# Kernel tuning notes

Measured on AMD Instinct MI355X. Metric: run time of the kernel, lower is better.

Reference implementation:

```python
import jax, jax.numpy as jnp
from jax import lax
import numpy as np

N = 10000      # nodes
T = 60         # lookback window
F = 16         # features per timestep
HL = 256       # lstm hidden dim
GH = 8         # gat heads
GC = 64        # gat out channels per head
GD = GH * GC   # 512 concat dim
FH = 512       # fusion hidden
E = 320000     # edges (before self loops)


def _lstm_layer(x, w_ih, w_hh, b_ih, b_hh):
    # x: [T, N, in] -> hidden sequence [T, N, HL]; torch gate order i,f,g,o
    n = x.shape[1]
    h0 = jnp.zeros((n, HL), x.dtype)
    def step(carry, xt):
        h, c = carry
        g = xt @ w_ih.T + h @ w_hh.T + b_ih + b_hh
        i, f, gg, o = jnp.split(g, 4, axis=-1)
        c = jax.nn.sigmoid(f) * c + jax.nn.sigmoid(i) * jnp.tanh(gg)
        h = jax.nn.sigmoid(o) * jnp.tanh(c)
        return (h, c), h
    _, hs = lax.scan(step, (h0, h0), x)
    return hs


def _gatv2(x, src, dst, ea, wl, bl, wr, br, we, att, bias):
    # GATv2Conv (concat=True, edge_dim=1, negative_slope=0.2); self loops already in src/dst/ea
    n = x.shape[0]
    xl = (x @ wl + bl).reshape(n, GH, GC)   # lin_l (source / x_j)
    xr = (x @ wr + br).reshape(n, GH, GC)   # lin_r (target / x_i)
    ee = (ea @ we).reshape(-1, GH, GC)      # lin_edge (bias=False)
    m = jax.nn.leaky_relu(xl[src] + xr[dst] + ee, 0.2)      # [E', GH, GC]
    logits = jnp.einsum('ehc,hc->eh', m, att)               # [E', GH]
    mx = jax.ops.segment_max(logits, dst, num_segments=n)
    ex = jnp.exp(logits - mx[dst])
    den = jax.ops.segment_sum(ex, dst, num_segments=n)
    alpha = ex / den[dst]                                   # softmax over in-edges per node
    out = jax.ops.segment_sum(xl[src] * alpha[..., None], dst, num_segments=n)
    return out.reshape(n, GD) + bias


def setup_inputs():
    key = jax.random.key(0)
    ks = jax.random.split(key, 20)
    f32 = jnp.float32
    def nrm(k, shp, fan):
        return jax.random.normal(k, shp, f32) * (1.0 / np.sqrt(fan))
    return {
        "x_seq": jax.random.normal(ks[0], (N, T, F), f32),
        "edge_index": jax.random.randint(ks[1], (2, E), 0, N, jnp.int32),
        "edge_attr": jax.random.uniform(ks[2], (E, 1), dtype=f32),
        "w_ih0": nrm(ks[3], (4 * HL, F), HL), "w_hh0": nrm(ks[4], (4 * HL, HL), HL),
        "b_ih0": jnp.zeros((4 * HL,), f32), "b_hh0": jnp.zeros((4 * HL,), f32),
        "w_ih1": nrm(ks[5], (4 * HL, HL), HL), "w_hh1": nrm(ks[6], (4 * HL, HL), HL),
        "b_ih1": jnp.zeros((4 * HL,), f32), "b_hh1": jnp.zeros((4 * HL,), f32),
        "g0_wl": nrm(ks[7], (HL, GD), HL), "g0_bl": jnp.zeros((GD,), f32),
        "g0_wr": nrm(ks[8], (HL, GD), HL), "g0_br": jnp.zeros((GD,), f32),
        "g0_we": nrm(ks[9], (1, GD), 1),
        "g0_att": nrm(ks[10], (GH, GC), GC), "g0_bias": jnp.zeros((GD,), f32),
        "g1_wl": nrm(ks[11], (GD, GD), GD), "g1_bl": jnp.zeros((GD,), f32),
        "g1_wr": nrm(ks[12], (GD, GD), GD), "g1_br": jnp.zeros((GD,), f32),
        "g1_we": nrm(ks[13], (1, GD), 1),
        "g1_att": nrm(ks[14], (GH, GC), GC), "g1_bias": jnp.zeros((GD,), f32),
        "fc1_w": nrm(ks[15], (HL + GD, FH), HL + GD), "fc1_b": jnp.zeros((FH,), f32),
        "fc2_w": nrm(ks[16], (FH, 1), FH), "fc2_b": jnp.zeros((1,), f32),
    }


def reference(x_seq, edge_index, edge_attr,
              w_ih0, w_hh0, b_ih0, b_hh0, w_ih1, w_hh1, b_ih1, b_hh1,
              g0_wl, g0_bl, g0_wr, g0_br, g0_we, g0_att, g0_bias,
              g1_wl, g1_bl, g1_wr, g1_br, g1_we, g1_att, g1_bias,
              fc1_w, fc1_b, fc2_w, fc2_b):
    # 2-layer LSTM encoder, take last timestep hidden (dropout off: eval mode)
    xt = jnp.transpose(x_seq, (1, 0, 2))            # [T, N, F]
    h1 = _lstm_layer(xt, w_ih0, w_hh0, b_ih0, b_hh0)
    h2 = _lstm_layer(h1, w_ih1, w_hh1, b_ih1, b_hh1)
    node = h2[-1]                                    # [N, HL]
    # add self loops; fill edge_attr for loops with mean (PyG default fill_value='mean')
    loop = jnp.arange(N, dtype=edge_index.dtype)
    src = jnp.concatenate([edge_index[0], loop])
    dst = jnp.concatenate([edge_index[1], loop])
    ea = jnp.concatenate([edge_attr, jnp.broadcast_to(edge_attr.mean(axis=0), (N, 1))], axis=0)
    g = jax.nn.elu(_gatv2(node, src, dst, ea, g0_wl, g0_bl, g0_wr, g0_br, g0_we, g0_att, g0_bias))
    g = jax.nn.elu(_gatv2(g, src, dst, ea, g1_wl, g1_bl, g1_wr, g1_br, g1_we, g1_att, g1_bias))
    fused = jnp.concatenate([node, g], axis=1)       # [N, HL+GD]
    h = jax.nn.relu(fused @ fc1_w + fc1_b)
    return h @ fc2_w + fc2_b                         # [N, 1]
```

## Files before the change

### kernel.cpp

```cpp
#include <hip/hip_runtime.h>

#define DEV __device__ __forceinline__

typedef _Float16 f16;
typedef _Float16 f16x8 __attribute__((ext_vector_type(8)));
typedef _Float16 f16x2 __attribute__((ext_vector_type(2)));
typedef float f32x4 __attribute__((ext_vector_type(4)));

DEV float sigmoidf_(float x) { return 1.0f / (1.0f + __expf(-x)); }
DEV float tanhf2_(float x)   { return 1.0f - 2.0f / (__expf(2.0f * x) + 1.0f); }

DEV void load_lds16(const void* g, void* l) {
    __builtin_amdgcn_global_load_lds(
        (const __attribute__((address_space(1))) char*)(const char*)g,
        (__attribute__((address_space(3))) char*)(unsigned int)(unsigned long long)(char*)l,
        16, 0, 0);
}

DEV int swz(int row, int ck) { return ck ^ (row & 3) ^ ((row >> 2) & 3); }

__global__ void prep_w0_kernel(const float* __restrict__ wih,
                               const float* __restrict__ whh,
                               f16* __restrict__ dst) {
    int idx = blockIdx.x * 256 + threadIdx.x;
    if (idx >= 1024 * 320) return;
    int rd = idx / 320, k = idx - rd * 320;
    int T = rd >> 7, p = rd & 127;
    int u = T * 32 + ((p >> 6) & 1) * 16 + (p & 15);
    int g = (p >> 4) & 3;
    int src = g * 256 + u;
    float v;
    if (k < 16)        v = wih[src * 16 + k];
    else if (k < 272)  v = whh[src * 256 + (k - 16)];
    else               v = 0.f;
    dst[idx] = (f16)v;
}

__global__ void prep_w1_kernel(const float* __restrict__ wih,
                               const float* __restrict__ whh,
                               f16* __restrict__ dst) {
    int idx = blockIdx.x * 256 + threadIdx.x;
    if (idx >= 1024 * 512) return;
    int rd = idx >> 9, k = idx & 511;
    int T = rd >> 7, p = rd & 127;
    int u = T * 32 + ((p >> 6) & 1) * 16 + (p & 15);
    int g = (p >> 4) & 3;
    int src = g * 256 + u;
    float v = (k < 256) ? wih[src * 256 + k] : whh[src * 256 + (k - 256)];
    dst[idx] = (f16)v;
}

__global__ void prep_bias4_kernel(const float* __restrict__ bi,
                                  const float* __restrict__ bh,
                                  float* __restrict__ dst) {
    int idx = blockIdx.x * 256 + threadIdx.x;
    if (idx >= 1024) return;
    int u = idx >> 2, g = idx & 3;
    dst[idx] = bi[g * 256 + u] + bh[g * 256 + u];
}

__global__ void prep_wt_kernel(const float* __restrict__ src, f16* __restrict__ dst,
                               int K, int N) {
    int idx = blockIdx.x * 256 + threadIdx.x;
    if (idx >= K * N) return;
    int n = idx / K, k = idx - n * K;
    dst[idx] = (f16)src[(size_t)k * N + n];
}

__global__ void prep_x0_kernel(const float* __restrict__ x_seq, f16* __restrict__ A0,
                               int Nn) {
    int idx = blockIdx.x * 256 + threadIdx.x;
    if (idx >= Nn * 16) return;
    int m = idx >> 4, f = idx & 15;
    A0[(size_t)m * 320 + f] = (f16)x_seq[(size_t)m * 960 + f];
}

DEV void lstm_step_core(
    f16* __restrict__ sA, f16* __restrict__ sB,
    int bx, int by,
    const f16* __restrict__ A, int lda, int K,
    const f16* __restrict__ Wt,
    const float* __restrict__ bias4,
    float* __restrict__ c_state,
    f16* __restrict__ hA, int ldhA, int offhA,
    f16* __restrict__ hB, int ldhB, int offhB,
    const float* __restrict__ xsrc, int tnext,
    int M)
{
    const int tid = threadIdx.x;
    const int w = tid >> 6, lane = tid & 63;
    const int m0 = bx * 128, n0 = by * 128;
    const int arow = lane >> 2;
    const int achk = swz(arow, lane & 3) * 8;
    const int frow = lane & 15, l4 = lane >> 4;
    const int fsl = swz(frow, l4) * 8;
    const int wr = (w >> 1) * 64, wc = (w & 1) * 64;

    const int u = by * 32 + (w & 1) * 16 + (lane & 15);
    const int rbase = m0 + wr + (lane >> 4) * 4;
    float cold[4][4];
#pragma unroll
    for (int i = 0; i < 4; ++i)
#pragma unroll
        for (int r = 0; r < 4; ++r)
            cold[i][r] = c_state[(size_t)(rbase + i * 16 + r) * 256 + u];

    f32x4 acc[4][4] = {};

    for (int k0 = 0; k0 < K; k0 += 64) {
        __syncthreads();
#pragma unroll
        for (int half = 0; half < 2; ++half) {
#pragma unroll
            for (int c = 0; c < 2; ++c) {
                int R = c * 64 + w * 16;
                load_lds16(A + (size_t)(m0 + R + arow) * lda + k0 + half * 32 + achk,
                           sA + half * 4096 + R * 32);
                load_lds16(Wt + (size_t)(n0 + R + arow) * K + k0 + half * 32 + achk,
                           sB + half * 4096 + R * 32);
            }
        }
        __syncthreads();
#pragma unroll
        for (int half = 0; half < 2; ++half) {
            f16x8 af[4], bf[4];
#pragma unroll
            for (int i = 0; i < 4; ++i)
                af[i] = *(const f16x8*)&sA[half * 4096 + (wr + i * 16 + frow) * 32 + fsl];
#pragma unroll
            for (int j = 0; j < 4; ++j)
                bf[j] = *(const f16x8*)&sB[half * 4096 + (wc + j * 16 + frow) * 32 + fsl];
#pragma unroll
            for (int i = 0; i < 4; ++i)
#pragma unroll
                for (int j = 0; j < 4; ++j)
                    acc[i][j] = __builtin_amdgcn_mfma_f32_16x16x32_f16(af[i], bf[j], acc[i][j], 0, 0, 0);
        }
    }

    const float4 bb = *(const float4*)&bias4[u * 4];
#pragma unroll
    for (int i = 0; i < 4; ++i) {
#pragma unroll
        for (int r = 0; r < 4; ++r) {
            int m = rbase + i * 16 + r;
            if (m < M) {
                float gi = sigmoidf_(acc[i][0][r] + bb.x);
                float gf = sigmoidf_(acc[i][1][r] + bb.y);
                float gg = tanhf2_(acc[i][2][r] + bb.z);
                float go = sigmoidf_(acc[i][3][r] + bb.w);
                float cn = gf * cold[i][r] + gi * gg;
                c_state[(size_t)m * 256 + u] = cn;
                f16 h = (f16)(go * tanhf2_(cn));
                hA[(size_t)m * ldhA + offhA + u] = h;
                if (hB) hB[(size_t)m * ldhB + offhB + u] = h;
            }
        }
    }
    if (xsrc && by == 0) {
        int row = tid >> 1, fb = (tid & 1) * 8;
        int m = m0 + row;
        if (m < M) {
            const float* xp = xsrc + (size_t)m * 960 + tnext * 16 + fb;
            f16* dp = hB + (size_t)m * ldhB + fb;
#pragma unroll
            for (int q = 0; q < 8; ++q) dp[q] = (f16)xp[q];
        }
    }
}

__global__ __launch_bounds__(256) void lstm_mfma_kernel(
    const f16* __restrict__ A, int lda, int K,
    const f16* __restrict__ Wt, const float* __restrict__ bias4,
    float* __restrict__ c_state,
    f16* __restrict__ hA, int ldhA, int offhA,
    f16* __restrict__ hB, int ldhB, int offhB,
    const float* __restrict__ xsrc, int tnext, int M, int mtiles)
{
    __shared__ __align__(16) f16 sA[2 * 4096];
    __shared__ __align__(16) f16 sB[2 * 4096];
    const int l = blockIdx.x;
    const int xcd = l & 7, q = l >> 3;
    const int y = q & 7, xhi = q >> 3;
    const int x = xhi * 8 + xcd;
    if (x >= mtiles) return;
    lstm_step_core(sA, sB, x, y, A, lda, K, Wt, bias4, c_state,
                   hA, ldhA, offhA, hB, ldhB, offhB, xsrc, tnext, M);
}

__global__ __launch_bounds__(256) void lstm_dual_kernel(
    const f16* __restrict__ A1, const f16* __restrict__ W1t,
    const float* __restrict__ b41, float* __restrict__ c1,
    f16* __restrict__ h1A, int ldh1A, int offh1A,
    const f16* __restrict__ A0, const f16* __restrict__ W0t,
    const float* __restrict__ b40, float* __restrict__ c0,
    f16* __restrict__ h0A, int ldh0A, int offh0A,
    f16* __restrict__ h0B, int ldh0B, int offh0B,
    const float* __restrict__ xsrc, int tnext, int M, int mtiles)
{
    __shared__ __align__(16) f16 sA[2 * 4096];
    __shared__ __align__(16) f16 sB[2 * 4096];
    const int l = blockIdx.x;
    const int xcd = l & 7, q = l >> 3;
    const int yz = q & 15, xhi = q >> 4;
    const int x = xhi * 8 + xcd;
    if (x >= mtiles) return;
    const int y = yz & 7, z = yz >> 3;
    if (z == 0)
        lstm_step_core(sA, sB, x, y, A1, 512, 512, W1t, b41, c1,
                       h1A, ldh1A, offh1A, nullptr, 0, 0, nullptr, 0, M);
    else
        lstm_step_core(sA, sB, x, y, A0, 320, 320, W0t, b40, c0,
                       h0A, ldh0A, offh0A, h0B, ldh0B, offh0B, xsrc, tnext, M);
}

__global__ __launch_bounds__(256) void gemm16_kernel(
    const f16* __restrict__ A, int lda,
    const f16* __restrict__ Bt, int K,
    const float* __restrict__ bias,
    f16* __restrict__ C16, float* __restrict__ C32, int ldc,
    int act, int M)
{
    __shared__ __align__(16) f16 sA[128 * 32];
    __shared__ __align__(16) f16 sB[128 * 32];
    const int tid = threadIdx.x;
    const int w = tid >> 6, lane = tid & 63;
    const int m0 = blockIdx.x * 128, n0 = blockIdx.y * 128;
    const int arow = lane >> 2;
    const int achk = swz(arow, lane & 3) * 8;
    const int frow = lane & 15, l4 = lane >> 4;
    const int fsl = swz(frow, l4) * 8;
    const int wr = (w >> 1) * 64, wcn = (w & 1) * 64;

    f32x4 acc[4][4] = {};

    for (int k0 = 0; k0 < K; k0 += 32) {
        __syncthreads();
#pragma unroll
        for (int c = 0; c < 2; ++c) {
            int R = c * 64 + w * 16;
            load_lds16(A + (size_t)(m0 + R + arow) * lda + k0 + achk, sA + R * 32);
            load_lds16(Bt + (size_t)(n0 + R + arow) * K + k0 + achk, sB + R * 32);
        }
        __syncthreads();
        f16x8 af[4], bf[4];
#pragma unroll
        for (int i = 0; i < 4; ++i)
            af[i] = *(const f16x8*)&sA[(wr + i * 16 + frow) * 32 + fsl];
#pragma unroll
        for (int j = 0; j < 4; ++j)
            bf[j] = *(const f16x8*)&sB[(wcn + j * 16 + frow) * 32 + fsl];
#pragma unroll
        for (int i = 0; i < 4; ++i)
#pragma unroll
            for (int j = 0; j < 4; ++j)
                acc[i][j] = __builtin_amdgcn_mfma_f32_16x16x32_f16(af[i], bf[j], acc[i][j], 0, 0, 0);
    }

    const int rbase = m0 + wr + (lane >> 4) * 4;
#pragma unroll
    for (int i = 0; i < 4; ++i) {
#pragma unroll
        for (int r = 0; r < 4; ++r) {
            int m = rbase + i * 16 + r;
            if (m >= M) continue;
#pragma unroll
            for (int j = 0; j < 4; ++j) {
                int n = n0 + wcn + j * 16 + (lane & 15);
                float v = acc[i][j][r] + bias[n];
                if (act == 1) v = fmaxf(v, 0.f);
                if (C16) C16[(size_t)m * ldc + n] = (f16)v;
                else     C32[(size_t)m * ldc + n] = v;
            }
        }
    }
}

__global__ __launch_bounds__(256) void gemm16_dual_kernel(
    const f16* __restrict__ A, int lda,
    const f16* __restrict__ Btl, const f16* __restrict__ Btr, int K,
    const float* __restrict__ biasl, const float* __restrict__ biasr,
    f16* __restrict__ Cl, f16* __restrict__ Cr, int ldc, int M)
{
    __shared__ __align__(16) f16 sA[128 * 32];
    __shared__ __align__(16) f16 sB[128 * 32];
    const int side = blockIdx.y >> 2;
    const f16* Bt = side ? Btr : Btl;
    const float* bias = side ? biasr : biasl;
    f16* C16 = side ? Cr : Cl;
    const int tid = threadIdx.x;
    const int w = tid >> 6, lane = tid & 63;
    const int m0 = blockIdx.x * 128, n0 = (blockIdx.y & 3) * 128;
    const int arow = lane >> 2;
    const int achk = swz(arow, lane & 3) * 8;
    const int frow = lane & 15, l4 = lane >> 4;
    const int fsl = swz(frow, l4) * 8;
    const int wr = (w >> 1) * 64, wcn = (w & 1) * 64;

    f32x4 acc[4][4] = {};

    for (int k0 = 0; k0 < K; k0 += 32) {
        __syncthreads();
#pragma unroll
        for (int c = 0; c < 2; ++c) {
            int R = c * 64 + w * 16;
            load_lds16(A + (size_t)(m0 + R + arow) * lda + k0 + achk, sA + R * 32);
            load_lds16(Bt + (size_t)(n0 + R + arow) * K + k0 + achk, sB + R * 32);
        }
        __syncthreads();
        f16x8 af[4], bf[4];
#pragma unroll
        for (int i = 0; i < 4; ++i)
            af[i] = *(const f16x8*)&sA[(wr + i * 16 + frow) * 32 + fsl];
#pragma unroll
        for (int j = 0; j < 4; ++j)
            bf[j] = *(const f16x8*)&sB[(wcn + j * 16 + frow) * 32 + fsl];
#pragma unroll
        for (int i = 0; i < 4; ++i)
#pragma unroll
            for (int j = 0; j < 4; ++j)
                acc[i][j] = __builtin_amdgcn_mfma_f32_16x16x32_f16(af[i], bf[j], acc[i][j], 0, 0, 0);
    }

    const int rbase = m0 + wr + (lane >> 4) * 4;
#pragma unroll
    for (int i = 0; i < 4; ++i) {
#pragma unroll
        for (int r = 0; r < 4; ++r) {
            int m = rbase + i * 16 + r;
            if (m >= M) continue;
#pragma unroll
            for (int j = 0; j < 4; ++j) {
                int n = n0 + wcn + j * 16 + (lane & 15);
                float v = acc[i][j][r] + bias[n];
                C16[(size_t)m * ldc + n] = (f16)v;
            }
        }
    }
}

__global__ void mean_sum_kernel(const float* __restrict__ a, int n, float* __restrict__ out) {
    __shared__ float s[256];
    float loc = 0.f;
    for (int i = blockIdx.x * 256 + threadIdx.x; i < n; i += gridDim.x * 256) loc += a[i];
    s[threadIdx.x] = loc;
    __syncthreads();
    for (int off = 128; off; off >>= 1) {
        if (threadIdx.x < off) s[threadIdx.x] += s[threadIdx.x + off];
        __syncthreads();
    }
    if (threadIdx.x == 0) atomicAdd(out, s[0]);
}

__global__ void hist_kernel(const int* __restrict__ ei, int Ne, int Nn,
                            int* __restrict__ counts) {
    int e = blockIdx.x * 256 + threadIdx.x;
    if (e >= Ne + Nn) return;
    int d = (e < Ne) ? ei[Ne + e] : (e - Ne);
    atomicAdd(&counts[d], 1);
}

__global__ void scan_kernel(const int* __restrict__ counts, int* __restrict__ offsets, int n) {
    __shared__ int s[256];
    int tid = threadIdx.x;
    int chunk = (n + 255) / 256;
    int b = tid * chunk;
    int loc = 0;
    for (int j = 0; j < chunk; ++j) { int i = b + j; if (i < n) loc += counts[i]; }
    s[tid] = loc;
    __syncthreads();
    for (int off = 1; off < 256; off <<= 1) {
        int v = (tid >= off) ? s[tid - off] : 0;
        __syncthreads();
        s[tid] += v;
        __syncthreads();
    }
    int run = (tid == 0) ? 0 : s[tid - 1];
    for (int j = 0; j < chunk; ++j) {
        int i = b + j;
        if (i < n) { offsets[i] = run; run += counts[i]; }
    }
    if (tid == 255) offsets[n] = run;
}

__global__ void scatter_kernel(const int* __restrict__ ei, const float* __restrict__ ea,
                               const float* __restrict__ sump, float inv_ne, int Ne, int Nn,
                               int* __restrict__ cursor, int* __restrict__ src_sorted,
                               float* __restrict__ ea_sorted) {
    int e = blockIdx.x * 256 + threadIdx.x;
    if (e >= Ne + Nn) return;
    int s, d; float a;
    if (e < Ne) { s = ei[e]; d = ei[Ne + e]; a = ea[e]; }
    else        { s = e - Ne; d = s; a = sump[0] * inv_ne; }
    int pos = atomicAdd(&cursor[d], 1);
    src_sorted[pos] = s;
    ea_sorted[pos] = a;
}

__global__ __launch_bounds__(256) void gat_aggregate_kernel(
    const f16* __restrict__ xl, const f16* __restrict__ xr,
    const float* __restrict__ we, const float* __restrict__ att,
    const float* __restrict__ bias,
    const int* __restrict__ offsets, const int* __restrict__ src_sorted,
    const float* __restrict__ ea_sorted,
    float* __restrict__ logit_buf, f16* __restrict__ out, int ldo, int N)
{
    __shared__ float s_xr[512], s_we[512], s_att[512];
    __shared__ float s_wmax[32], s_mx[8], s_den[8], s_rden[8];
    __shared__ float s_alpha[256];
    __shared__ int s_src[32];
    const int i = blockIdx.x;
    const int tid = threadIdx.x;
    s_xr[tid]       = (float)xr[(size_t)i * 512 + tid];
    s_xr[tid + 256] = (float)xr[(size_t)i * 512 + tid + 256];
    s_we[tid] = we[tid]; s_we[tid + 256] = we[tid + 256];
    s_att[tid] = att[tid]; s_att[tid + 256] = att[tid + 256];
    if (tid < 8) s_den[tid] = 0.f;
    __syncthreads();

    const int beg = offsets[i], end = offsets[i + 1];
    const int w = tid >> 6, lane = tid & 63;

    float wm[4] = {-1e30f, -1e30f, -1e30f, -1e30f};
    for (int e = beg + w; e < end; e += 4) {
        int s = src_sorted[e];
        float a = ea_sorted[e];
        float part[4];
#pragma unroll
        for (int cc = 0; cc < 4; ++cc) {
            int col = cc * 128 + lane * 2;
            f16x2 xv = *(const f16x2*)&xl[(size_t)s * 512 + col];
            float v0 = (float)xv.x + s_xr[col]     + a * s_we[col];
            float v1 = (float)xv.y + s_xr[col + 1] + a * s_we[col + 1];
            v0 = (v0 > 0.f) ? v0 : 0.2f * v0;
            v1 = (v1 > 0.f) ? v1 : 0.2f * v1;
            part[cc] = v0 * s_att[col] + v1 * s_att[col + 1];
        }
#pragma unroll
        for (int off = 16; off; off >>= 1)
#pragma unroll
            for (int cc = 0; cc < 4; ++cc) part[cc] += __shfl_xor(part[cc], off);
        if ((lane & 31) == 0) {
            int hb = lane >> 5;
#pragma unroll
            for (int cc = 0; cc < 4; ++cc) {
                logit_buf[(size_t)e * 8 + 2 * cc + hb] = part[cc];
                wm[cc] = fmaxf(wm[cc], part[cc]);
            }
        }
    }
    if ((lane & 31) == 0) {
        int hb = lane >> 5;
#pragma unroll
        for (int cc = 0; cc < 4; ++cc) s_wmax[w * 8 + 2 * cc + hb] = wm[cc];
    }
    __syncthreads();
    if (tid < 8) {
        float m = fmaxf(fmaxf(s_wmax[tid], s_wmax[8 + tid]),
                        fmaxf(s_wmax[16 + tid], s_wmax[24 + tid]));
        s_mx[tid] = m;
    }
    __syncthreads();

    for (int e = beg + tid; e < end; e += 256) {
#pragma unroll
        for (int h = 0; h < 8; ++h) {
            float ex = __expf(logit_buf[(size_t)e * 8 + h] - s_mx[h]);
            logit_buf[(size_t)e * 8 + h] = ex;
            atomicAdd(&s_den[h], ex);
        }
    }
    __syncthreads();
    if (tid < 8) s_rden[tid] = 1.f / s_den[tid];
    __syncthreads();

    float acc0 = 0.f, acc1 = 0.f;
    const int c2 = tid * 2, hh = tid >> 5;
    for (int chunk = beg; chunk < end; chunk += 32) {
        int cnt = min(32, end - chunk);
        if (tid < cnt) s_src[tid] = src_sorted[chunk + tid];
        int eo = tid >> 3, hq = tid & 7;
        if (eo < cnt) s_alpha[tid] = logit_buf[(size_t)(chunk + eo) * 8 + hq] * s_rden[hq];
        __syncthreads();
        for (int j = 0; j < cnt; ++j) {
            int s = s_src[j];
            f16x2 xv = *(const f16x2*)&xl[(size_t)s * 512 + c2];
            float al = s_alpha[j * 8 + hh];
            acc0 += al * (float)xv.x;
            acc1 += al * (float)xv.y;
        }
        __syncthreads();
    }
    float v0 = acc0 + bias[c2];
    float v1 = acc1 + bias[c2 + 1];
    v0 = (v0 > 0.f) ? v0 : __expf(v0) - 1.f;
    v1 = (v1 > 0.f) ? v1 : __expf(v1) - 1.f;
    f16x2 ov; ov.x = (f16)v0; ov.y = (f16)v1;
    *(f16x2*)&out[(size_t)i * ldo + c2] = ov;
}

__global__ void fc2_kernel(const float* __restrict__ H, const float* __restrict__ w,
                           const float* __restrict__ b, float* __restrict__ out, int N) {
    int wv = threadIdx.x >> 6, lane = threadIdx.x & 63;
    int node = blockIdx.x * 4 + wv;
    if (node >= N) return;
    float s = 0.f;
#pragma unroll
    for (int j = 0; j < 8; ++j)
        s += H[(size_t)node * 512 + j * 64 + lane] * w[j * 64 + lane];
#pragma unroll
    for (int off = 32; off; off >>= 1) s += __shfl_xor(s, off, 64);
    if (lane == 0) out[node] = s + b[0];
}

extern "C" void kernel_launch(void* const* d_in, const int* in_sizes, int n_in,
                              void* d_out, int out_size, void* d_ws, size_t ws_size,
                              hipStream_t stream) {
    const float* x_seq     = (const float*)d_in[0];
    const int*   edge_index= (const int*)d_in[1];
    const float* edge_attr = (const float*)d_in[2];
    const float* w_ih0 = (const float*)d_in[3];
    const float* w_hh0 = (const float*)d_in[4];
    const float* b_ih0 = (const float*)d_in[5];
    const float* b_hh0 = (const float*)d_in[6];
    const float* w_ih1 = (const float*)d_in[7];
    const float* w_hh1 = (const float*)d_in[8];
    const float* b_ih1 = (const float*)d_in[9];
    const float* b_hh1 = (const float*)d_in[10];
    const float* g0_wl = (const float*)d_in[11];
    const float* g0_bl = (const float*)d_in[12];
    const float* g0_wr = (const float*)d_in[13];
    const float* g0_br = (const float*)d_in[14];
    const float* g0_we = (const float*)d_in[15];
    const float* g0_att= (const float*)d_in[16];
    const float* g0_bias=(const float*)d_in[17];
    const float* g1_wl = (const float*)d_in[18];
    const float* g1_bl = (const float*)d_in[19];
    const float* g1_wr = (const float*)d_in[20];
    const float* g1_br = (const float*)d_in[21];
    const float* g1_we = (const float*)d_in[22];
    const float* g1_att= (const float*)d_in[23];
    const float* g1_bias=(const float*)d_in[24];
    const float* fc1_w = (const float*)d_in[25];
    const float* fc1_b = (const float*)d_in[26];
    const float* fc2_w = (const float*)d_in[27];
    const float* fc2_b = (const float*)d_in[28];
    float* out = (float*)d_out;

    const int Nn = in_sizes[0] / (60 * 16);
    const int Ne = in_sizes[1] / 2;
    const int Etot = Ne + Nn;
    const int MT = (Nn + 127) / 128;
    const int Mpad = MT * 128;
    const int MTpad8 = ((MT + 7) / 8) * 8;

    size_t off = 0;
    auto alloc = [&](size_t bytes) -> void* {
        void* r = (char*)d_ws + off;
        off += (bytes + 255) & ~(size_t)255;
        return r;
    };
    f16* W0t   = (f16*)alloc((size_t)1024 * 320 * 2);
    f16* W1t   = (f16*)alloc((size_t)1024 * 512 * 2);
    float* b40 = (float*)alloc(1024 * 4);
    float* b41 = (float*)alloc(1024 * 4);
    f16* Wg0l  = (f16*)alloc((size_t)512 * 256 * 2);
    f16* Wg0r  = (f16*)alloc((size_t)512 * 256 * 2);
    f16* Wg1l  = (f16*)alloc((size_t)512 * 512 * 2);
    f16* Wg1r  = (f16*)alloc((size_t)512 * 512 * 2);
    f16* Wfc1  = (f16*)alloc((size_t)512 * 768 * 2);
    f16* A0b[2]; A0b[0] = (f16*)alloc((size_t)Mpad * 320 * 2);
                 A0b[1] = (f16*)alloc((size_t)Mpad * 320 * 2);
    f16* A1b[2]; A1b[0] = (f16*)alloc((size_t)Mpad * 512 * 2);
                 A1b[1] = (f16*)alloc((size_t)Mpad * 512 * 2);
    float* c0  = (float*)alloc((size_t)Mpad * 256 * 4);
    float* c1  = (float*)alloc((size_t)Mpad * 256 * 4);
    f16* fused = (f16*)alloc((size_t)Mpad * 768 * 2);
    f16* xlbuf = (f16*)alloc((size_t)Mpad * 512 * 2);
    f16* xrbuf = (f16*)alloc((size_t)Mpad * 512 * 2);
    f16* gbuf  = (f16*)alloc((size_t)Mpad * 512 * 2);
    float* hfc1= (float*)alloc((size_t)Mpad * 512 * 4);
    float* logit_buf = (float*)alloc((size_t)Etot * 8 * 4);
    int* counts  = (int*)alloc((size_t)Nn * 4);
    int* offsets = (int*)alloc((size_t)(Nn + 1) * 4);
    int* cursor  = (int*)alloc((size_t)Nn * 4);
    int* src_sorted = (int*)alloc((size_t)Etot * 4);
    float* ea_sorted = (float*)alloc((size_t)Etot * 4);
    float* meanp = (float*)alloc(256);

    prep_w0_kernel<<<dim3((1024 * 320 + 255) / 256), 256, 0, stream>>>(w_ih0, w_hh0, W0t);
    prep_w1_kernel<<<dim3((1024 * 512 + 255) / 256), 256, 0, stream>>>(w_ih1, w_hh1, W1t);
    prep_bias4_kernel<<<dim3(4), 256, 0, stream>>>(b_ih0, b_hh0, b40);
    prep_bias4_kernel<<<dim3(4), 256, 0, stream>>>(b_ih1, b_hh1, b41);
    prep_wt_kernel<<<dim3((256 * 512 + 255) / 256), 256, 0, stream>>>(g0_wl, Wg0l, 256, 512);
    prep_wt_kernel<<<dim3((256 * 512 + 255) / 256), 256, 0, stream>>>(g0_wr, Wg0r, 256, 512);
    prep_wt_kernel<<<dim3((512 * 512 + 255) / 256), 256, 0, stream>>>(g1_wl, Wg1l, 512, 512);
    prep_wt_kernel<<<dim3((512 * 512 + 255) / 256), 256, 0, stream>>>(g1_wr, Wg1r, 512, 512);
    prep_wt_kernel<<<dim3((768 * 512 + 255) / 256), 256, 0, stream>>>(fc1_w, Wfc1, 768, 512);
    hipMemsetAsync(A0b[0], 0, (size_t)Mpad * 320 * 2, stream);
    hipMemsetAsync(A0b[1], 0, (size_t)Mpad * 320 * 2, stream);
    hipMemsetAsync(A1b[0], 0, (size_t)Mpad * 512 * 2, stream);
    hipMemsetAsync(c0, 0, (size_t)Mpad * 256 * 4, stream);
    hipMemsetAsync(c1, 0, (size_t)Mpad * 256 * 4, stream);
    prep_x0_kernel<<<dim3((Nn * 16 + 255) / 256), 256, 0, stream>>>(x_seq, A0b[0], Nn);

    hipMemsetAsync(meanp, 0, 4, stream);
    hipMemsetAsync(counts, 0, (size_t)Nn * 4, stream);
    mean_sum_kernel<<<dim3(256), 256, 0, stream>>>(edge_attr, Ne, meanp);
    hist_kernel<<<dim3((Etot + 255) / 256), 256, 0, stream>>>(edge_index, Ne, Nn, counts);
    scan_kernel<<<dim3(1), 256, 0, stream>>>(counts, offsets, Nn);
    hipMemcpyAsync(cursor, offsets, (size_t)Nn * 4, hipMemcpyDeviceToDevice, stream);
    scatter_kernel<<<dim3((Etot + 255) / 256), 256, 0, stream>>>(
        edge_index, edge_attr, meanp, 1.0f / (float)Ne, Ne, Nn, cursor, src_sorted, ea_sorted);

    const int solo_grid = MTpad8 * 8;
    const int dual_grid = MTpad8 * 16;
    lstm_mfma_kernel<<<dim3(solo_grid), 256, 0, stream>>>(
        A0b[0], 320, 320, W0t, b40, c0,
        A1b[0], 512, 0,
        A0b[1], 320, 16,
        x_seq, 1, Nn, MT);
    for (int k = 0; k < 59; ++k) {
        lstm_dual_kernel<<<dim3(dual_grid), 256, 0, stream>>>(
            A1b[k & 1], W1t, b41, c1,
            A1b[(k + 1) & 1], 512, 256,
            A0b[(k + 1) & 1], W0t, b40, c0,
            A1b[(k + 1) & 1], 512, 0,
            A0b[k & 1], 320, 16,
            (k + 1 < 59) ? x_seq : nullptr, k + 2, Nn, MT);
    }
    lstm_mfma_kernel<<<dim3(solo_grid), 256, 0, stream>>>(
        A1b[1], 512, 512, W1t, b41, c1,
        fused, 768, 0,
        nullptr, 0, 0,
        nullptr, 0, Nn, MT);

    gemm16_dual_kernel<<<dim3(MT, 8), 256, 0, stream>>>(
        fused, 768, Wg0l, Wg0r, 256, g0_bl, g0_br, xlbuf, xrbuf, 512, Nn);
    gat_aggregate_kernel<<<dim3(Nn), 256, 0, stream>>>(
        xlbuf, xrbuf, g0_we, g0_att, g0_bias, offsets, src_sorted, ea_sorted,
        logit_buf, gbuf, 512, Nn);

    gemm16_dual_kernel<<<dim3(MT, 8), 256, 0, stream>>>(
        gbuf, 512, Wg1l, Wg1r, 512, g1_bl, g1_br, xlbuf, xrbuf, 512, Nn);
    gat_aggregate_kernel<<<dim3(Nn), 256, 0, stream>>>(
        xlbuf, xrbuf, g1_we, g1_att, g1_bias, offsets, src_sorted, ea_sorted,
        logit_buf, fused + 256, 768, Nn);

    gemm16_kernel<<<dim3(MT, 4), 256, 0, stream>>>(
        fused, 768, Wfc1, 768, fc1_b, nullptr, hfc1, 512, 1, Nn);
    fc2_kernel<<<dim3((Nn + 3) / 4), 256, 0, stream>>>(hfc1, fc2_w, fc2_b, out, Nn);
}
```

Before: 3.363 ms.

## Double-buffer LDS tiles to overlap global loads with MFMA in GEMM kernels

The LSTM step core and both FP16 GEMM kernels now use a two-stage LDS ping-pong over 32-wide K chunks. The next chunk's global→LDS loads are issued right after a single barrier, before computing on the current chunk, so load latency overlaps with MFMA work and there is one barrier per chunk instead of two. The cost is double the LDS footprint in the GEMM kernels, which may lower occupancy. Because the barrier also waits on outstanding vector memory, the overlap only covers one chunk of compute.

```diff
diff --git a/kernel.cpp b/kernel.cpp
--- a/kernel.cpp
+++ b/kernel.cpp
@@ -75,6 +75,37 @@
     A0[(size_t)m * 320 + f] = (f16)x_seq[(size_t)m * 960 + f];
 }
 
+DEV void tile_load_chunk(const f16* __restrict__ A, int lda,
+                         const f16* __restrict__ Bt, int K,
+                         int m0, int n0, int k0,
+                         f16* __restrict__ sA, f16* __restrict__ sB,
+                         int w, int arow, int achk)
+{
+#pragma unroll
+    for (int c = 0; c < 2; ++c) {
+        int R = c * 64 + w * 16;
+        load_lds16(A + (size_t)(m0 + R + arow) * lda + k0 + achk, sA + R * 32);
+        load_lds16(Bt + (size_t)(n0 + R + arow) * K + k0 + achk, sB + R * 32);
+    }
+}
+
+DEV void tile_compute_chunk(const f16* __restrict__ sA, const f16* __restrict__ sB,
+                            f32x4 (&acc)[4][4], int wr, int wc, int frow, int fsl)
+{
+    f16x8 af[4], bf[4];
+#pragma unroll
+    for (int i = 0; i < 4; ++i)
+        af[i] = *(const f16x8*)&sA[(wr + i * 16 + frow) * 32 + fsl];
+#pragma unroll
+    for (int j = 0; j < 4; ++j)
+        bf[j] = *(const f16x8*)&sB[(wc + j * 16 + frow) * 32 + fsl];
+#pragma unroll
+    for (int i = 0; i < 4; ++i)
+#pragma unroll
+        for (int j = 0; j < 4; ++j)
+            acc[i][j] = __builtin_amdgcn_mfma_f32_16x16x32_f16(af[i], bf[j], acc[i][j], 0, 0, 0);
+}
+
 DEV void lstm_step_core(
     f16* __restrict__ sA, f16* __restrict__ sB,
     int bx, int by,
@@ -106,36 +137,18 @@
             cold[i][r] = c_state[(size_t)(rbase + i * 16 + r) * 256 + u];
 
     f32x4 acc[4][4] = {};
-
-    for (int k0 = 0; k0 < K; k0 += 64) {
-        __syncthreads();
-#pragma unroll
-        for (int half = 0; half < 2; ++half) {
-#pragma unroll
-            for (int c = 0; c < 2; ++c) {
-                int R = c * 64 + w * 16;
-                load_lds16(A + (size_t)(m0 + R + arow) * lda + k0 + half * 32 + achk,
-                           sA + half * 4096 + R * 32);
-                load_lds16(Wt + (size_t)(n0 + R + arow) * K + k0 + half * 32 + achk,
-                           sB + half * 4096 + R * 32);
-            }
-        }
-        __syncthreads();
-#pragma unroll
-        for (int half = 0; half < 2; ++half) {
-            f16x8 af[4], bf[4];
-#pragma unroll
-            for (int i = 0; i < 4; ++i)
-                af[i] = *(const f16x8*)&sA[half * 4096 + (wr + i * 16 + frow) * 32 + fsl];
-#pragma unroll
-            for (int j = 0; j < 4; ++j)
-                bf[j] = *(const f16x8*)&sB[half * 4096 + (wc + j * 16 + frow) * 32 + fsl];
-#pragma unroll
-            for (int i = 0; i < 4; ++i)
-#pragma unroll
-                for (int j = 0; j < 4; ++j)
-                    acc[i][j] = __builtin_amdgcn_mfma_f32_16x16x32_f16(af[i], bf[j], acc[i][j], 0, 0, 0);
-        }
+    const int nch = K >> 5;
+
+    tile_load_chunk(A, lda, Wt, K, m0, n0, 0, sA, sB, w, arow, achk);
+    for (int kc = 0; kc < nch; ++kc) {
+        __syncthreads();
+        const int cur = (kc & 1) * 4096;
+        if (kc + 1 < nch) {
+            const int nxt = ((kc + 1) & 1) * 4096;
+            tile_load_chunk(A, lda, Wt, K, m0, n0, (kc + 1) * 32,
+                            sA + nxt, sB + nxt, w, arow, achk);
+        }
+        tile_compute_chunk(sA + cur, sB + cur, acc, wr, wc, frow, fsl);
     }
 
     const float4 bb = *(const float4*)&bias4[u * 4];
@@ -221,8 +234,8 @@
     f16* __restrict__ C16, float* __restrict__ C32, int ldc,
     int act, int M)
 {
-    __shared__ __align__(16) f16 sA[128 * 32];
-    __shared__ __align__(16) f16 sB[128 * 32];
+    __shared__ __align__(16) f16 sA[2 * 4096];
+    __shared__ __align__(16) f16 sB[2 * 4096];
     const int tid = threadIdx.x;
     const int w = tid >> 6, lane = tid & 63;
     const int m0 = blockIdx.x * 128, n0 = blockIdx.y * 128;
@@ -233,28 +246,18 @@
     const int wr = (w >> 1) * 64, wcn = (w & 1) * 64;
 
     f32x4 acc[4][4] = {};
-
-    for (int k0 = 0; k0 < K; k0 += 32) {
-        __syncthreads();
-#pragma unroll
-        for (int c = 0; c < 2; ++c) {
-            int R = c * 64 + w * 16;
-            load_lds16(A + (size_t)(m0 + R + arow) * lda + k0 + achk, sA + R * 32);
-            load_lds16(Bt + (size_t)(n0 + R + arow) * K + k0 + achk, sB + R * 32);
-        }
-        __syncthreads();
-        f16x8 af[4], bf[4];
-#pragma unroll
-        for (int i = 0; i < 4; ++i)
-            af[i] = *(const f16x8*)&sA[(wr + i * 16 + frow) * 32 + fsl];
-#pragma unroll
-        for (int j = 0; j < 4; ++j)
-            bf[j] = *(const f16x8*)&sB[(wcn + j * 16 + frow) * 32 + fsl];
-#pragma unroll
-        for (int i = 0; i < 4; ++i)
-#pragma unroll
-            for (int j = 0; j < 4; ++j)
-                acc[i][j] = __builtin_amdgcn_mfma_f32_16x16x32_f16(af[i], bf[j], acc[i][j], 0, 0, 0);
+    const int nch = K >> 5;
+
+    tile_load_chunk(A, lda, Bt, K, m0, n0, 0, sA, sB, w, arow, achk);
+    for (int kc = 0; kc < nch; ++kc) {
+        __syncthreads();
+        const int cur = (kc & 1) * 4096;
+        if (kc + 1 < nch) {
+            const int nxt = ((kc + 1) & 1) * 4096;
+            tile_load_chunk(A, lda, Bt, K, m0, n0, (kc + 1) * 32,
+                            sA + nxt, sB + nxt, w, arow, achk);
+        }
+        tile_compute_chunk(sA + cur, sB + cur, acc, wr, wcn, frow, fsl);
     }
 
     const int rbase = m0 + wr + (lane >> 4) * 4;
@@ -282,8 +285,8 @@
     const float* __restrict__ biasl, const float* __restrict__ biasr,
     f16* __restrict__ Cl, f16* __restrict__ Cr, int ldc, int M)
 {
-    __shared__ __align__(16) f16 sA[128 * 32];
-    __shared__ __align__(16) f16 sB[128 * 32];
+    __shared__ __align__(16) f16 sA[2 * 4096];
+    __shared__ __align__(16) f16 sB[2 * 4096];
     const int side = blockIdx.y >> 2;
     const f16* Bt = side ? Btr : Btl;
     const float* bias = side ? biasr : biasl;
@@ -298,28 +301,18 @@
     const int wr = (w >> 1) * 64, wcn = (w & 1) * 64;
 
     f32x4 acc[4][4] = {};
-
-    for (int k0 = 0; k0 < K; k0 += 32) {
-        __syncthreads();
-#pragma unroll
-        for (int c = 0; c < 2; ++c) {
-            int R = c * 64 + w * 16;
-            load_lds16(A + (size_t)(m0 + R + arow) * lda + k0 + achk, sA + R * 32);
-            load_lds16(Bt + (size_t)(n0 + R + arow) * K + k0 + achk, sB + R * 32);
-        }
-        __syncthreads();
-        f16x8 af[4], bf[4];
-#pragma unroll
-        for (int i = 0; i < 4; ++i)
-            af[i] = *(const f16x8*)&sA[(wr + i * 16 + frow) * 32 + fsl];
-#pragma unroll
-        for (int j = 0; j < 4; ++j)
-            bf[j] = *(const f16x8*)&sB[(wcn + j * 16 + frow) * 32 + fsl];
-#pragma unroll
-        for (int i = 0; i < 4; ++i)
-#pragma unroll
-            for (int j = 0; j < 4; ++j)
-                acc[i][j] = __builtin_amdgcn_mfma_f32_16x16x32_f16(af[i], bf[j], acc[i][j], 0, 0, 0);
+    const int nch = K >> 5;
+
+    tile_load_chunk(A, lda, Bt, K, m0, n0, 0, sA, sB, w, arow, achk);
+    for (int kc = 0; kc < nch; ++kc) {
+        __syncthreads();
+        const int cur = (kc & 1) * 4096;
+        if (kc + 1 < nch) {
+            const int nxt = ((kc + 1) & 1) * 4096;
+            tile_load_chunk(A, lda, Bt, K, m0, n0, (kc + 1) * 32,
+                            sA + nxt, sB + nxt, w, arow, achk);
+        }
+        tile_compute_chunk(sA + cur, sB + cur, acc, wr, wcn, frow, fsl);
     }
 
     const int rbase = m0 + wr + (lane >> 4) * 4;
```

Measured after the change: 3.130 ms. 6.9% less time.
